# Kernel optimization log

Hardware: AMD Instinct MI355X
Metric: run time of the kernel (lower is better)

Reference implementation:

```python
import jax, jax.numpy as jnp
import numpy as np

GAMMA = 2.0
EPS = 1e-06
LAMBDA_DISTANCE = 1.0
LAMBDA_NORMAL = 0.01
LAMBDA_LAPLACIAN = 0.1
CLS = 1


def vertex_normals(v, f, eps=EPS):
    # v: [N,3], f: [F,3] int. Scatter face normals to vertices, then normalize.
    fv = v[f]  # [F,3,3]
    fn = jnp.cross(fv[:, 1] - fv[:, 0], fv[:, 2] - fv[:, 0])  # [F,3]
    vn = jnp.zeros_like(v)
    vn = vn.at[f[:, 0]].add(fn).at[f[:, 1]].add(fn).at[f[:, 2]].add(fn)
    norm = jnp.maximum(jnp.linalg.norm(vn, axis=-1, keepdims=True), eps)
    return vn / norm


def squared_cdist(a, b):
    # [Na,3] x [Nb,3] -> squared euclidean distances [Na,Nb] (clamped >= 0)
    a2 = jnp.sum(a * a, axis=1)[:, None]
    b2 = jnp.sum(b * b, axis=1)[None, :]
    d2 = a2 + b2 - 2.0 * (a @ b.T)
    return jnp.maximum(d2, 0.0)


def sample_binary_targets(label, v, cls=CLS):
    # Nearest-neighbor grid_sample, align_corners=True, padding zeros.
    # grid = 2*v - 1 -> voxel index = round(v * (size-1)); v[:,0]->W, v[:,1]->H, v[:,2]->D.
    D, H, W = label.shape[2], label.shape[3], label.shape[4]
    ix = jnp.round(v[:, 0] * (W - 1)).astype(jnp.int32)
    iy = jnp.round(v[:, 1] * (H - 1)).astype(jnp.int32)
    iz = jnp.round(v[:, 2] * (D - 1)).astype(jnp.int32)
    inb = (ix >= 0) & (ix < W) & (iy >= 0) & (iy < H) & (iz >= 0) & (iz < D)
    ixc = jnp.clip(ix, 0, W - 1)
    iyc = jnp.clip(iy, 0, H - 1)
    izc = jnp.clip(iz, 0, D - 1)
    vals = (label[0, 0, izc, iyc, ixc] == cls).astype(jnp.float32)
    return jnp.where(inb, vals, 0.0)


def spatial_consistency_loss(rel_pos, targets, gamma=GAMMA, eps=EPS):
    p = jnp.clip(rel_pos, eps, 1.0 - eps)
    pos = targets > 0.5
    pc = jnp.sum(pos).astype(p.dtype)
    tot = jnp.asarray(p.shape[0], p.dtype)
    nc = tot - pc
    alpha = nc / (tot + eps)
    lpos = -alpha * jnp.power(1.0 - p, gamma) * jnp.log(p)
    lneg = -(1.0 - alpha) * jnp.power(p, gamma) * jnp.log(1.0 - p)
    return jnp.sum(jnp.where(pos, lpos, lneg)) / (tot + eps)


def laplacian_uniform(v, f):
    # Uniform mesh Laplacian smoothing: || mean(neighbors) - v ||, averaged.
    i = jnp.concatenate([f[:, 0], f[:, 1], f[:, 2], f[:, 1], f[:, 2], f[:, 0]])
    j = jnp.concatenate([f[:, 1], f[:, 2], f[:, 0], f[:, 0], f[:, 1], f[:, 2]])
    nsum = jnp.zeros_like(v).at[i].add(v[j])
    deg = jnp.zeros((v.shape[0],), v.dtype).at[i].add(1.0)
    lap = nsum / jnp.maximum(deg, 1.0)[:, None] - v
    return jnp.mean(jnp.linalg.norm(lap, axis=1))


def loss_forward(pred_vertices, relative_positions, gt_vertices, pred_faces, gt_faces, label):
    gt_v = jax.lax.stop_gradient(gt_vertices)  # gt comes from label volume; detached in original
    gt_normals = vertex_normals(gt_v, gt_faces)
    # spatial (focal-style) loss
    targets = sample_binary_targets(label, pred_vertices)
    spatial = spatial_consistency_loss(relative_positions, targets)
    # chamfer-style squared surface distance
    d2 = squared_cdist(pred_vertices, gt_v)  # [Np,Ng]
    distance = jnp.mean(jnp.min(d2, axis=1)) + jnp.mean(jnp.min(d2, axis=0))
    # normal consistency vs nearest gt vertex
    pred_normals = vertex_normals(pred_vertices, pred_faces)
    nearest = jnp.argmin(d2, axis=1)
    normal = jnp.mean((pred_normals - gt_normals[nearest]) ** 2)
    # uniform laplacian smoothing
    laplacian = laplacian_uniform(pred_vertices, pred_faces)
    total = spatial + LAMBDA_DISTANCE * distance + LAMBDA_NORMAL * normal + LAMBDA_LAPLACIAN * laplacian
    return total


def setup_inputs() -> dict:
    key = jax.random.key(0)
    k1, k2, k3, k4, k5, k6 = jax.random.split(key, 6)
    Np, Ng = 8192, 12000
    pred_vertices = jax.random.uniform(k1, (Np, 3), dtype=jnp.float32)
    relative_positions = jax.random.uniform(k2, (Np,), dtype=jnp.float32)
    gt_vertices = jax.random.uniform(k3, (Ng, 3), dtype=jnp.float32)
    pred_faces = jax.random.randint(k4, (2 * Np, 3), 0, Np, dtype=jnp.int32)
    gt_faces = jax.random.randint(k5, (2 * Ng, 3), 0, Ng, dtype=jnp.int32)
    label = jax.random.randint(k6, (1, 1, 96, 96, 96), 0, 2, dtype=jnp.int32)
    return {"pred_vertices": pred_vertices, "relative_positions": relative_positions,
            "gt_vertices": gt_vertices, "pred_faces": pred_faces,
            "gt_faces": gt_faces, "label": label}


def reference(pred_vertices, relative_positions, gt_vertices, pred_faces, gt_faces, label):
    return loss_forward(pred_vertices, relative_positions, gt_vertices, pred_faces, gt_faces, label)
```

## Files before the change

### kernel.cpp

```cpp
#include <hip/hip_runtime.h>
#include <math.h>

#define NP 8192
#define NG 12000
#define NFP 16384
#define NFG 24000
#define EPSF 1e-6f

static constexpr size_t OFF_ROWMIN = 0;
static constexpr size_t OFF_COLMIN = 65536;
static constexpr size_t OFF_GTN    = 113664;
static constexpr size_t OFF_PNN    = 257664;
static constexpr size_t OFF_NSUM   = 355968;
static constexpr size_t OFF_DEG    = 454272;
static constexpr size_t OFF_SCAL   = 487040;
#define N_ZERO 93352

__global__ __launch_bounds__(256) void init_kernel(unsigned long long* __restrict__ rowmin,
                                                   unsigned* __restrict__ colmin,
                                                   float* __restrict__ zero) {
    int i = blockIdx.x * 256 + threadIdx.x;
    if (i < NP) rowmin[i] = 0xFFFFFFFFFFFFFFFFULL;
    if (i < NG) colmin[i] = 0x7f800000u;
    if (i < N_ZERO) zero[i] = 0.0f;
}

#define ROW_GROUPS 8
#define ROW_CHUNKS 64
#define ROW_CH 188
#define ROW_BLOCKS (ROW_GROUPS*ROW_CHUNKS)
#define COL_GROUPS 12
#define COL_CHUNKS 43
#define COL_CH 192
#define COL_BLOCKS (COL_GROUPS*COL_CHUNKS)
#define CD_BLOCKS (ROW_BLOCKS + COL_BLOCKS)
#define FACE_BLOCKS ((NFG + NFP + 255) / 256)

__global__ __launch_bounds__(256) void mega_kernel(const float* __restrict__ pred,
                                                   const int* __restrict__ pf,
                                                   const float* __restrict__ gt,
                                                   const int* __restrict__ gf,
                                                   unsigned long long* __restrict__ rowmin,
                                                   unsigned* __restrict__ colmin,
                                                   float* __restrict__ gtn,
                                                   float* __restrict__ pnn,
                                                   float* __restrict__ nsum,
                                                   float* __restrict__ deg) {
    __shared__ float4 s[COL_CH];
    int b = blockIdx.x;
    if (b < ROW_BLOCKS) {
        int group = b >> 6;
        int chunk = b & 63;
        int gbase = chunk * ROW_CH;
        for (int j = threadIdx.x; j < ROW_CH; j += 256) {
            int gj = gbase + j;
            if (gj < NG) {
                float x = gt[3*gj], y = gt[3*gj+1], z = gt[3*gj+2];
                s[j] = make_float4(x, y, z, fmaf(x,x, fmaf(y,y, z*z)));
            } else {
                s[j] = make_float4(0.f, 0.f, 0.f, 3.0e38f);
            }
        }
        __syncthreads();
        int pv0 = group * 1024 + threadIdx.x;
        float cx[4], cy[4], cz[4], a2[4], best[4];
        int bi[4];
        #pragma unroll
        for (int k = 0; k < 4; ++k) {
            int pv = pv0 + 256*k;
            float x = pred[3*pv], y = pred[3*pv+1], z = pred[3*pv+2];
            a2[k] = fmaf(x,x, fmaf(y,y, z*z));
            cx[k] = -2.0f*x; cy[k] = -2.0f*y; cz[k] = -2.0f*z;
            best[k] = 3.0e38f; bi[k] = 0;
        }
        #pragma unroll 4
        for (int j = 0; j < ROW_CH; ++j) {
            float4 q = s[j];
            #pragma unroll
            for (int k = 0; k < 4; ++k) {
                float t = fmaf(cx[k], q.x, fmaf(cy[k], q.y, fmaf(cz[k], q.z, q.w)));
                if (t < best[k]) { best[k] = t; bi[k] = gbase + j; }
            }
        }
        #pragma unroll
        for (int k = 0; k < 4; ++k) {
            float d2 = fmaxf(a2[k] + best[k], 0.0f);
            unsigned long long key =
                ((unsigned long long)__float_as_uint(d2) << 32) | (unsigned)bi[k];
            atomicMin(&rowmin[pv0 + 256*k], key);
        }
    } else if (b < CD_BLOCKS) {
        int bb = b - ROW_BLOCKS;
        int group = bb / COL_CHUNKS;
        int chunk = bb % COL_CHUNKS;
        int pbase = chunk * COL_CH;
        for (int j = threadIdx.x; j < COL_CH; j += 256) {
            int pj = pbase + j;
            if (pj < NP) {
                float x = pred[3*pj], y = pred[3*pj+1], z = pred[3*pj+2];
                s[j] = make_float4(x, y, z, fmaf(x,x, fmaf(y,y, z*z)));
            } else {
                s[j] = make_float4(0.f, 0.f, 0.f, 3.0e38f);
            }
        }
        __syncthreads();
        int gv0 = group * 1024 + threadIdx.x;
        float cx[4], cy[4], cz[4], a2[4], best[4];
        #pragma unroll
        for (int k = 0; k < 4; ++k) {
            int gv = gv0 + 256*k;
            float x = 0.f, y = 0.f, z = 0.f;
            if (gv < NG) { x = gt[3*gv]; y = gt[3*gv+1]; z = gt[3*gv+2]; }
            a2[k] = fmaf(x,x, fmaf(y,y, z*z));
            cx[k] = -2.0f*x; cy[k] = -2.0f*y; cz[k] = -2.0f*z;
            best[k] = 3.0e38f;
        }
        #pragma unroll 4
        for (int j = 0; j < COL_CH; ++j) {
            float4 q = s[j];
            #pragma unroll
            for (int k = 0; k < 4; ++k) {
                float t = fmaf(cx[k], q.x, fmaf(cy[k], q.y, fmaf(cz[k], q.z, q.w)));
                best[k] = fminf(best[k], t);
            }
        }
        #pragma unroll
        for (int k = 0; k < 4; ++k) {
            int gv = gv0 + 256*k;
            if (gv < NG) {
                float d2 = fmaxf(a2[k] + best[k], 0.0f);
                atomicMin(&colmin[gv], __float_as_uint(d2));
            }
        }
    } else {
        int t = (b - CD_BLOCKS) * 256 + threadIdx.x;
        if (t < NFG) {
            int i0 = gf[3*t], i1 = gf[3*t+1], i2 = gf[3*t+2];
            float ax = gt[3*i0], ay = gt[3*i0+1], az = gt[3*i0+2];
            float bx = gt[3*i1], by = gt[3*i1+1], bz = gt[3*i1+2];
            float cx = gt[3*i2], cy = gt[3*i2+1], cz = gt[3*i2+2];
            float ux = bx-ax, uy = by-ay, uz = bz-az;
            float wx = cx-ax, wy = cy-ay, wz = cz-az;
            float nx = uy*wz - uz*wy, ny = uz*wx - ux*wz, nz = ux*wy - uy*wx;
            atomicAdd(&gtn[3*i0+0], nx); atomicAdd(&gtn[3*i0+1], ny); atomicAdd(&gtn[3*i0+2], nz);
            atomicAdd(&gtn[3*i1+0], nx); atomicAdd(&gtn[3*i1+1], ny); atomicAdd(&gtn[3*i1+2], nz);
            atomicAdd(&gtn[3*i2+0], nx); atomicAdd(&gtn[3*i2+1], ny); atomicAdd(&gtn[3*i2+2], nz);
        } else if (t < NFG + NFP) {
            int u = t - NFG;
            int i0 = pf[3*u], i1 = pf[3*u+1], i2 = pf[3*u+2];
            float ax = pred[3*i0], ay = pred[3*i0+1], az = pred[3*i0+2];
            float bx = pred[3*i1], by = pred[3*i1+1], bz = pred[3*i1+2];
            float cx = pred[3*i2], cy = pred[3*i2+1], cz = pred[3*i2+2];
            float ux = bx-ax, uy = by-ay, uz = bz-az;
            float wx = cx-ax, wy = cy-ay, wz = cz-az;
            float nx = uy*wz - uz*wy, ny = uz*wx - ux*wz, nz = ux*wy - uy*wx;
            atomicAdd(&pnn[3*i0+0], nx); atomicAdd(&pnn[3*i0+1], ny); atomicAdd(&pnn[3*i0+2], nz);
            atomicAdd(&pnn[3*i1+0], nx); atomicAdd(&pnn[3*i1+1], ny); atomicAdd(&pnn[3*i1+2], nz);
            atomicAdd(&pnn[3*i2+0], nx); atomicAdd(&pnn[3*i2+1], ny); atomicAdd(&pnn[3*i2+2], nz);
            atomicAdd(&nsum[3*i0+0], bx+cx); atomicAdd(&nsum[3*i0+1], by+cy); atomicAdd(&nsum[3*i0+2], bz+cz);
            atomicAdd(&nsum[3*i1+0], cx+ax); atomicAdd(&nsum[3*i1+1], cy+ay); atomicAdd(&nsum[3*i1+2], cz+az);
            atomicAdd(&nsum[3*i2+0], ax+bx); atomicAdd(&nsum[3*i2+1], ay+by); atomicAdd(&nsum[3*i2+2], az+bz);
            atomicAdd(&deg[i0], 2.0f); atomicAdd(&deg[i1], 2.0f); atomicAdd(&deg[i2], 2.0f);
        }
    }
}

__device__ __forceinline__ float wave_sum(float x) {
    #pragma unroll
    for (int o = 32; o > 0; o >>= 1) x += __shfl_down(x, o, 64);
    return x;
}

#define FIN_PRED_BLOCKS 32
#define FIN_COL_BLOCKS 47
#define FIN_TOTAL (FIN_PRED_BLOCKS + FIN_COL_BLOCKS)
__global__ __launch_bounds__(256) void finalize_kernel(const float* __restrict__ pred,
                                                       const float* __restrict__ relpos,
                                                       const int* __restrict__ label,
                                                       const unsigned long long* __restrict__ rowmin,
                                                       const unsigned* __restrict__ colmin,
                                                       const float* __restrict__ pnn,
                                                       const float* __restrict__ gtn,
                                                       const float* __restrict__ nsum,
                                                       const float* __restrict__ deg,
                                                       float* __restrict__ scal,
                                                       unsigned* __restrict__ ticket,
                                                       float* __restrict__ out) {
    if (blockIdx.x < FIN_PRED_BLOCKS) {
        int v = blockIdx.x * 256 + threadIdx.x;
        unsigned long long key = rowmin[v];
        float dmin = __uint_as_float((unsigned)(key >> 32));
        int nearest = (int)(unsigned)(key & 0xffffffffu);
        float px = pred[3*v], py = pred[3*v+1], pz = pred[3*v+2];

        float ax = pnn[3*v], ay = pnn[3*v+1], az = pnn[3*v+2];
        float an = fmaxf(sqrtf(ax*ax + ay*ay + az*az), EPSF);
        float gx = gtn[3*nearest], gy = gtn[3*nearest+1], gz = gtn[3*nearest+2];
        float gn = fmaxf(sqrtf(gx*gx + gy*gy + gz*gz), EPSF);
        float nx = ax/an - gx/gn, ny = ay/an - gy/gn, nz = az/an - gz/gn;
        float sse = nx*nx + ny*ny + nz*nz;

        float d = fmaxf(deg[v], 1.0f);
        float lx = nsum[3*v]/d - px, ly = nsum[3*v+1]/d - py, lz = nsum[3*v+2]/d - pz;
        float lapn = sqrtf(lx*lx + ly*ly + lz*lz);

        int ix = (int)rintf(px * 95.0f), iy = (int)rintf(py * 95.0f), iz = (int)rintf(pz * 95.0f);
        bool inb = (ix >= 0) & (ix < 96) & (iy >= 0) & (iy < 96) & (iz >= 0) & (iz < 96);
        int ixc = min(max(ix, 0), 95), iyc = min(max(iy, 0), 95), izc = min(max(iz, 0), 95);
        bool pos = inb && (label[(izc*96 + iyc)*96 + ixc] == 1);

        float p = fminf(fmaxf(relpos[v], EPSF), 1.0f - EPSF);
        float om = 1.0f - p;
        float pcnt = 0.0f, sx = 0.0f, sy = 0.0f;
        if (pos) { pcnt = 1.0f; sx = om*om*logf(p); }
        else     { sy = p*p*logf(om); }

        float r0 = wave_sum(dmin);
        float r1 = wave_sum(sse);
        float r2 = wave_sum(lapn);
        float r3 = wave_sum(pcnt);
        float r4 = wave_sum(sx);
        float r5 = wave_sum(sy);
        if ((threadIdx.x & 63) == 0) {
            atomicAdd(&scal[0], r0);
            atomicAdd(&scal[5], r1);
            atomicAdd(&scal[6], r2);
            atomicAdd(&scal[2], r3);
            atomicAdd(&scal[3], r4);
            atomicAdd(&scal[4], r5);
        }
    } else {
        int gv = (blockIdx.x - FIN_PRED_BLOCKS) * 256 + threadIdx.x;
        float val = (gv < NG) ? __uint_as_float(colmin[gv]) : 0.0f;
        float r = wave_sum(val);
        if ((threadIdx.x & 63) == 0) atomicAdd(&scal[1], r);
    }

    __threadfence();
    __shared__ int is_last;
    if (threadIdx.x == 0) {
        unsigned t = atomicAdd(ticket, 1u);
        is_last = (t == FIN_TOTAL - 1) ? 1 : 0;
    }
    __syncthreads();
    if (is_last && threadIdx.x == 0) {
        float sum_row = atomicAdd(&scal[0], 0.0f);
        float sum_col = atomicAdd(&scal[1], 0.0f);
        float pc      = atomicAdd(&scal[2], 0.0f);
        float SX      = atomicAdd(&scal[3], 0.0f);
        float SY      = atomicAdd(&scal[4], 0.0f);
        float sse     = atomicAdd(&scal[5], 0.0f);
        float lap     = atomicAdd(&scal[6], 0.0f);
        float tot = (float)NP;
        float alpha = (tot - pc) / (tot + EPSF);
        float spatial = (-alpha * SX - (1.0f - alpha) * SY) / (tot + EPSF);
        float distance = sum_row / (float)NP + sum_col / (float)NG;
        float normal = sse / (float)(NP * 3);
        float lapm = lap / (float)NP;
        out[0] = spatial + 1.0f * distance + 0.01f * normal + 0.1f * lapm;
    }
}

extern "C" void kernel_launch(void* const* d_in, const int* in_sizes, int n_in,
                              void* d_out, int out_size, void* d_ws, size_t ws_size,
                              hipStream_t stream) {
    const float* pred   = (const float*)d_in[0];
    const float* relpos = (const float*)d_in[1];
    const float* gt     = (const float*)d_in[2];
    const int*   pfaces = (const int*)d_in[3];
    const int*   gfaces = (const int*)d_in[4];
    const int*   label  = (const int*)d_in[5];
    float* out = (float*)d_out;

    char* ws = (char*)d_ws;
    unsigned long long* rowmin = (unsigned long long*)(ws + OFF_ROWMIN);
    unsigned*           colmin = (unsigned*)(ws + OFF_COLMIN);
    float*              gtn    = (float*)(ws + OFF_GTN);
    float*              pnn    = (float*)(ws + OFF_PNN);
    float*              nsum   = (float*)(ws + OFF_NSUM);
    float*              deg    = (float*)(ws + OFF_DEG);
    float*              scal   = (float*)(ws + OFF_SCAL);
    unsigned*           ticket = (unsigned*)(ws + OFF_SCAL + 7*sizeof(float));

    hipLaunchKernelGGL(init_kernel, dim3((N_ZERO + 255) / 256), dim3(256), 0, stream,
                       rowmin, colmin, gtn);
    hipLaunchKernelGGL(mega_kernel, dim3(CD_BLOCKS + FACE_BLOCKS), dim3(256), 0, stream,
                       pred, pfaces, gt, gfaces, rowmin, colmin, gtn, pnn, nsum, deg);
    hipLaunchKernelGGL(finalize_kernel, dim3(FIN_TOTAL), dim3(256), 0, stream,
                       pred, relpos, label, rowmin, colmin, pnn, gtn, nsum, deg,
                       scal, ticket, out);
}
```

Measured before the change: 120.2 us.

## Replace atomicMin chamfer reduction with per-chunk partial buffers reduced in finalize

The chamfer row/column kernels now write per-chunk partial minima into large workspace buffers instead of doing global atomicMin, and the finalize kernel scans all chunks to reduce them. Each thread also handles 8 query points instead of 4 while the shared chunk is halved, which raises register reuse per shared-memory load. The init kernel no longer has to initialise the min buffers. In exchange, finalize reads about 12 MB of partial results, and the higher register count may lower occupancy.

New measurement: 134.6 us. 1.12x slower.

```diff
diff --git a/kernel.cpp b/kernel.cpp
--- a/kernel.cpp
+++ b/kernel.cpp
@@ -7,41 +7,38 @@
 #define NFG 24000
 #define EPSF 1e-6f
 
-static constexpr size_t OFF_ROWMIN = 0;
-static constexpr size_t OFF_COLMIN = 65536;
-static constexpr size_t OFF_GTN    = 113664;
-static constexpr size_t OFF_PNN    = 257664;
-static constexpr size_t OFF_NSUM   = 355968;
-static constexpr size_t OFF_DEG    = 454272;
-static constexpr size_t OFF_SCAL   = 487040;
-#define N_ZERO 93352
-
-__global__ __launch_bounds__(256) void init_kernel(unsigned long long* __restrict__ rowmin,
-                                                   unsigned* __restrict__ colmin,
-                                                   float* __restrict__ zero) {
-    int i = blockIdx.x * 256 + threadIdx.x;
-    if (i < NP) rowmin[i] = 0xFFFFFFFFFFFFFFFFULL;
-    if (i < NG) colmin[i] = 0x7f800000u;
-    if (i < N_ZERO) zero[i] = 0.0f;
-}
-
-#define ROW_GROUPS 8
-#define ROW_CHUNKS 64
-#define ROW_CH 188
+#define ROW_GROUPS 4
+#define ROW_CHUNKS 128
+#define ROW_CH 94
 #define ROW_BLOCKS (ROW_GROUPS*ROW_CHUNKS)
-#define COL_GROUPS 12
-#define COL_CHUNKS 43
-#define COL_CH 192
+#define COL_GROUPS 6
+#define COL_CHUNKS 86
+#define COL_CH 96
 #define COL_BLOCKS (COL_GROUPS*COL_CHUNKS)
 #define CD_BLOCKS (ROW_BLOCKS + COL_BLOCKS)
 #define FACE_BLOCKS ((NFG + NFP + 255) / 256)
+#define NGPAD (COL_GROUPS*2048)
+
+static constexpr size_t OFF_ROWPART = 0;
+static constexpr size_t OFF_COLPART = 8388608;
+static constexpr size_t OFF_GTN     = 12615680;
+static constexpr size_t OFF_PNN     = 12759680;
+static constexpr size_t OFF_NSUM    = 12857984;
+static constexpr size_t OFF_DEG     = 12956288;
+static constexpr size_t OFF_SCAL    = 12989056;
+#define N_ZERO 93352
+
+__global__ __launch_bounds__(256) void init_kernel(float* __restrict__ zero) {
+    int i = blockIdx.x * 256 + threadIdx.x;
+    if (i < N_ZERO) zero[i] = 0.0f;
+}
 
 __global__ __launch_bounds__(256) void mega_kernel(const float* __restrict__ pred,
                                                    const int* __restrict__ pf,
                                                    const float* __restrict__ gt,
                                                    const int* __restrict__ gf,
-                                                   unsigned long long* __restrict__ rowmin,
-                                                   unsigned* __restrict__ colmin,
+                                                   unsigned long long* __restrict__ rowpart,
+                                                   float* __restrict__ colpart,
                                                    float* __restrict__ gtn,
                                                    float* __restrict__ pnn,
                                                    float* __restrict__ nsum,
@@ -49,9 +46,20 @@
     __shared__ float4 s[COL_CH];
     int b = blockIdx.x;
     if (b < ROW_BLOCKS) {
-        int group = b >> 6;
-        int chunk = b & 63;
+        int group = b >> 7;
+        int chunk = b & 127;
         int gbase = chunk * ROW_CH;
+        int pv0 = group * 2048 + threadIdx.x;
+        float cx[8], cy[8], cz[8], a2[8], best[8];
+        int bi[8];
+        #pragma unroll
+        for (int k = 0; k < 8; ++k) {
+            int pv = pv0 + 256*k;
+            float x = pred[3*pv], y = pred[3*pv+1], z = pred[3*pv+2];
+            a2[k] = fmaf(x,x, fmaf(y,y, z*z));
+            cx[k] = -2.0f*x; cy[k] = -2.0f*y; cz[k] = -2.0f*z;
+            best[k] = 3.0e38f; bi[k] = 0;
+        }
         for (int j = threadIdx.x; j < ROW_CH; j += 256) {
             int gj = gbase + j;
             if (gj < NG) {
@@ -62,38 +70,37 @@
             }
         }
         __syncthreads();
-        int pv0 = group * 1024 + threadIdx.x;
-        float cx[4], cy[4], cz[4], a2[4], best[4];
-        int bi[4];
-        #pragma unroll
-        for (int k = 0; k < 4; ++k) {
-            int pv = pv0 + 256*k;
-            float x = pred[3*pv], y = pred[3*pv+1], z = pred[3*pv+2];
-            a2[k] = fmaf(x,x, fmaf(y,y, z*z));
-            cx[k] = -2.0f*x; cy[k] = -2.0f*y; cz[k] = -2.0f*z;
-            best[k] = 3.0e38f; bi[k] = 0;
-        }
-        #pragma unroll 4
+        #pragma unroll 2
         for (int j = 0; j < ROW_CH; ++j) {
             float4 q = s[j];
             #pragma unroll
-            for (int k = 0; k < 4; ++k) {
+            for (int k = 0; k < 8; ++k) {
                 float t = fmaf(cx[k], q.x, fmaf(cy[k], q.y, fmaf(cz[k], q.z, q.w)));
-                if (t < best[k]) { best[k] = t; bi[k] = gbase + j; }
-            }
-        }
-        #pragma unroll
-        for (int k = 0; k < 4; ++k) {
+                if (t < best[k]) { best[k] = t; bi[k] = j; }
+            }
+        }
+        #pragma unroll
+        for (int k = 0; k < 8; ++k) {
             float d2 = fmaxf(a2[k] + best[k], 0.0f);
-            unsigned long long key =
-                ((unsigned long long)__float_as_uint(d2) << 32) | (unsigned)bi[k];
-            atomicMin(&rowmin[pv0 + 256*k], key);
+            rowpart[(size_t)chunk * NP + pv0 + 256*k] =
+                ((unsigned long long)__float_as_uint(d2) << 32) | (unsigned)(gbase + bi[k]);
         }
     } else if (b < CD_BLOCKS) {
         int bb = b - ROW_BLOCKS;
         int group = bb / COL_CHUNKS;
         int chunk = bb % COL_CHUNKS;
         int pbase = chunk * COL_CH;
+        int gv0 = group * 2048 + threadIdx.x;
+        float cx[8], cy[8], cz[8], a2[8], best[8];
+        #pragma unroll
+        for (int k = 0; k < 8; ++k) {
+            int gv = gv0 + 256*k;
+            float x = 0.f, y = 0.f, z = 0.f;
+            if (gv < NG) { x = gt[3*gv]; y = gt[3*gv+1]; z = gt[3*gv+2]; }
+            a2[k] = fmaf(x,x, fmaf(y,y, z*z));
+            cx[k] = -2.0f*x; cy[k] = -2.0f*y; cz[k] = -2.0f*z;
+            best[k] = 3.0e38f;
+        }
         for (int j = threadIdx.x; j < COL_CH; j += 256) {
             int pj = pbase + j;
             if (pj < NP) {
@@ -104,33 +111,19 @@
             }
         }
         __syncthreads();
-        int gv0 = group * 1024 + threadIdx.x;
-        float cx[4], cy[4], cz[4], a2[4], best[4];
-        #pragma unroll
-        for (int k = 0; k < 4; ++k) {
-            int gv = gv0 + 256*k;
-            float x = 0.f, y = 0.f, z = 0.f;
-            if (gv < NG) { x = gt[3*gv]; y = gt[3*gv+1]; z = gt[3*gv+2]; }
-            a2[k] = fmaf(x,x, fmaf(y,y, z*z));
-            cx[k] = -2.0f*x; cy[k] = -2.0f*y; cz[k] = -2.0f*z;
-            best[k] = 3.0e38f;
-        }
-        #pragma unroll 4
+        #pragma unroll 2
         for (int j = 0; j < COL_CH; ++j) {
             float4 q = s[j];
             #pragma unroll
-            for (int k = 0; k < 4; ++k) {
+            for (int k = 0; k < 8; ++k) {
                 float t = fmaf(cx[k], q.x, fmaf(cy[k], q.y, fmaf(cz[k], q.z, q.w)));
                 best[k] = fminf(best[k], t);
             }
         }
         #pragma unroll
-        for (int k = 0; k < 4; ++k) {
-            int gv = gv0 + 256*k;
-            if (gv < NG) {
-                float d2 = fmaxf(a2[k] + best[k], 0.0f);
-                atomicMin(&colmin[gv], __float_as_uint(d2));
-            }
+        for (int k = 0; k < 8; ++k) {
+            float d2 = fmaxf(a2[k] + best[k], 0.0f);
+            colpart[(size_t)chunk * NGPAD + gv0 + 256*k] = d2;
         }
     } else {
         int t = (b - CD_BLOCKS) * 256 + threadIdx.x;
@@ -172,13 +165,13 @@
 }
 
 #define FIN_PRED_BLOCKS 32
-#define FIN_COL_BLOCKS 47
+#define FIN_COL_BLOCKS 48
 #define FIN_TOTAL (FIN_PRED_BLOCKS + FIN_COL_BLOCKS)
 __global__ __launch_bounds__(256) void finalize_kernel(const float* __restrict__ pred,
                                                        const float* __restrict__ relpos,
                                                        const int* __restrict__ label,
-                                                       const unsigned long long* __restrict__ rowmin,
-                                                       const unsigned* __restrict__ colmin,
+                                                       const unsigned long long* __restrict__ rowpart,
+                                                       const float* __restrict__ colpart,
                                                        const float* __restrict__ pnn,
                                                        const float* __restrict__ gtn,
                                                        const float* __restrict__ nsum,
@@ -188,7 +181,12 @@
                                                        float* __restrict__ out) {
     if (blockIdx.x < FIN_PRED_BLOCKS) {
         int v = blockIdx.x * 256 + threadIdx.x;
-        unsigned long long key = rowmin[v];
+        unsigned long long key = 0xFFFFFFFFFFFFFFFFULL;
+        #pragma unroll 4
+        for (int c = 0; c < ROW_CHUNKS; ++c) {
+            unsigned long long k2 = rowpart[(size_t)c * NP + v];
+            key = (k2 < key) ? k2 : key;
+        }
         float dmin = __uint_as_float((unsigned)(key >> 32));
         int nearest = (int)(unsigned)(key & 0xffffffffu);
         float px = pred[3*v], py = pred[3*v+1], pz = pred[3*v+2];
@@ -231,7 +229,11 @@
         }
     } else {
         int gv = (blockIdx.x - FIN_PRED_BLOCKS) * 256 + threadIdx.x;
-        float val = (gv < NG) ? __uint_as_float(colmin[gv]) : 0.0f;
+        float best = 3.4e38f;
+        #pragma unroll 4
+        for (int c = 0; c < COL_CHUNKS; ++c)
+            best = fminf(best, colpart[(size_t)c * NGPAD + gv]);
+        float val = (gv < NG) ? best : 0.0f;
         float r = wave_sum(val);
         if ((threadIdx.x & 63) == 0) atomicAdd(&scal[1], r);
     }
@@ -273,20 +275,20 @@
     float* out = (float*)d_out;
 
     char* ws = (char*)d_ws;
-    unsigned long long* rowmin = (unsigned long long*)(ws + OFF_ROWMIN);
-    unsigned*           colmin = (unsigned*)(ws + OFF_COLMIN);
-    float*              gtn    = (float*)(ws + OFF_GTN);
-    float*              pnn    = (float*)(ws + OFF_PNN);
-    float*              nsum   = (float*)(ws + OFF_NSUM);
-    float*              deg    = (float*)(ws + OFF_DEG);
-    float*              scal   = (float*)(ws + OFF_SCAL);
-    unsigned*           ticket = (unsigned*)(ws + OFF_SCAL + 7*sizeof(float));
+    unsigned long long* rowpart = (unsigned long long*)(ws + OFF_ROWPART);
+    float*              colpart = (float*)(ws + OFF_COLPART);
+    float*              gtn     = (float*)(ws + OFF_GTN);
+    float*              pnn     = (float*)(ws + OFF_PNN);
+    float*              nsum    = (float*)(ws + OFF_NSUM);
+    float*              deg     = (float*)(ws + OFF_DEG);
+    float*              scal    = (float*)(ws + OFF_SCAL);
+    unsigned*           ticket  = (unsigned*)(ws + OFF_SCAL + 7*sizeof(float));
 
     hipLaunchKernelGGL(init_kernel, dim3((N_ZERO + 255) / 256), dim3(256), 0, stream,
-                       rowmin, colmin, gtn);
+                       gtn);
     hipLaunchKernelGGL(mega_kernel, dim3(CD_BLOCKS + FACE_BLOCKS), dim3(256), 0, stream,
-                       pred, pfaces, gt, gfaces, rowmin, colmin, gtn, pnn, nsum, deg);
+                       pred, pfaces, gt, gfaces, rowpart, colpart, gtn, pnn, nsum, deg);
     hipLaunchKernelGGL(finalize_kernel, dim3(FIN_TOTAL), dim3(256), 0, stream,
-                       pred, relpos, label, rowmin, colmin, pnn, gtn, nsum, deg,
+                       pred, relpos, label, rowpart, colpart, pnn, gtn, nsum, deg,
                        scal, ticket, out);
 }
```

## Replace brute-force Chamfer distance with uniform grid nearest-neighbor search

Applied to the files above, without the earlier changes.

Replaces the all-pairs squared-distance min reductions with a 16^3 uniform grid. A single block builds cell histograms and prefix sums, a scatter pass buckets points into cell-sorted float4 arrays, and the finalize kernel queries each point by expanding Chebyshev shells until a distance bound proves the best is final. This removes O(Np*Ng) distance work at the cost of a serial single-block build, atomic scatter with nondeterministic order within cells, and divergent per-thread search loops. It relies on the coordinates being roughly uniform in [0,1].

Result: slower. 172.2 us (+43.3%).

```diff
diff --git a/kernel.cpp b/kernel.cpp
--- a/kernel.cpp
+++ b/kernel.cpp
@@ -7,133 +7,122 @@
 #define NFG 24000
 #define EPSF 1e-6f
 
-static constexpr size_t OFF_ROWMIN = 0;
-static constexpr size_t OFF_COLMIN = 65536;
-static constexpr size_t OFF_GTN    = 113664;
-static constexpr size_t OFF_PNN    = 257664;
-static constexpr size_t OFF_NSUM   = 355968;
-static constexpr size_t OFF_DEG    = 454272;
-static constexpr size_t OFF_SCAL   = 487040;
+#define GR 16
+#define NC (GR*GR*GR)
+#define HCELL 0.0625f
+
+static constexpr size_t OFF_STARTP = 0;
+static constexpr size_t OFF_CURP   = 16384;
+static constexpr size_t OFF_STARTG = 32768;
+static constexpr size_t OFF_CURG   = 49152;
+static constexpr size_t OFF_SORTP  = 65536;
+static constexpr size_t OFF_SORTG  = 196608;
+static constexpr size_t OFF_GTN    = 388608;
+static constexpr size_t OFF_PNN    = 532608;
+static constexpr size_t OFF_NSUM   = 630912;
+static constexpr size_t OFF_DEG    = 729216;
+static constexpr size_t OFF_SCAL   = 761984;
+static constexpr size_t OFF_TICKET = 762012;
 #define N_ZERO 93352
 
-__global__ __launch_bounds__(256) void init_kernel(unsigned long long* __restrict__ rowmin,
-                                                   unsigned* __restrict__ colmin,
-                                                   float* __restrict__ zero) {
-    int i = blockIdx.x * 256 + threadIdx.x;
-    if (i < NP) rowmin[i] = 0xFFFFFFFFFFFFFFFFULL;
-    if (i < NG) colmin[i] = 0x7f800000u;
-    if (i < N_ZERO) zero[i] = 0.0f;
-}
-
-#define ROW_GROUPS 8
-#define ROW_CHUNKS 64
-#define ROW_CH 188
-#define ROW_BLOCKS (ROW_GROUPS*ROW_CHUNKS)
-#define COL_GROUPS 12
-#define COL_CHUNKS 43
-#define COL_CH 192
-#define COL_BLOCKS (COL_GROUPS*COL_CHUNKS)
-#define CD_BLOCKS (ROW_BLOCKS + COL_BLOCKS)
+__device__ __forceinline__ int cell_of(float x) {
+    int c = (int)(x * (float)GR);
+    return min(max(c, 0), GR - 1);
+}
+
+__global__ __launch_bounds__(1024) void build_kernel(const float* __restrict__ pred,
+                                                     const float* __restrict__ gt,
+                                                     unsigned* __restrict__ startP,
+                                                     unsigned* __restrict__ curP,
+                                                     unsigned* __restrict__ startG,
+                                                     unsigned* __restrict__ curG,
+                                                     float* __restrict__ zero) {
+    if (blockIdx.x == 0) {
+        __shared__ unsigned hP[NC];
+        __shared__ unsigned hG[NC];
+        __shared__ unsigned ps[1024];
+        int t = threadIdx.x;
+        for (int i = t; i < NC; i += 1024) { hP[i] = 0u; hG[i] = 0u; }
+        __syncthreads();
+        for (int i = t; i < NP; i += 1024) {
+            int c = (cell_of(pred[3*i+2]) * GR + cell_of(pred[3*i+1])) * GR + cell_of(pred[3*i]);
+            atomicAdd(&hP[c], 1u);
+        }
+        for (int i = t; i < NG; i += 1024) {
+            int c = (cell_of(gt[3*i+2]) * GR + cell_of(gt[3*i+1])) * GR + cell_of(gt[3*i]);
+            atomicAdd(&hG[c], 1u);
+        }
+        __syncthreads();
+        {
+            unsigned a0 = hP[4*t], a1 = hP[4*t+1], a2 = hP[4*t+2], a3 = hP[4*t+3];
+            unsigned tsum = a0 + a1 + a2 + a3;
+            ps[t] = tsum; __syncthreads();
+            for (int off = 1; off < 1024; off <<= 1) {
+                unsigned v = (t >= off) ? ps[t - off] : 0u;
+                __syncthreads();
+                ps[t] += v;
+                __syncthreads();
+            }
+            unsigned ex = ps[t] - tsum;
+            hP[4*t] = ex; hP[4*t+1] = ex + a0; hP[4*t+2] = ex + a0 + a1; hP[4*t+3] = ex + a0 + a1 + a2;
+            __syncthreads();
+            for (int i = t; i < NC; i += 1024) { startP[i] = hP[i]; curP[i] = hP[i]; }
+            __syncthreads();
+        }
+        {
+            unsigned a0 = hG[4*t], a1 = hG[4*t+1], a2 = hG[4*t+2], a3 = hG[4*t+3];
+            unsigned tsum = a0 + a1 + a2 + a3;
+            ps[t] = tsum; __syncthreads();
+            for (int off = 1; off < 1024; off <<= 1) {
+                unsigned v = (t >= off) ? ps[t - off] : 0u;
+                __syncthreads();
+                ps[t] += v;
+                __syncthreads();
+            }
+            unsigned ex = ps[t] - tsum;
+            hG[4*t] = ex; hG[4*t+1] = ex + a0; hG[4*t+2] = ex + a0 + a1; hG[4*t+3] = ex + a0 + a1 + a2;
+            __syncthreads();
+            for (int i = t; i < NC; i += 1024) { startG[i] = hG[i]; curG[i] = hG[i]; }
+        }
+    } else {
+        int i = (blockIdx.x - 1) * 1024 + threadIdx.x;
+        if (i < N_ZERO) zero[i] = 0.0f;
+    }
+}
+
+#define SCAT_P_BLOCKS 32
+#define SCAT_G_BLOCKS 47
+#define SCAT_BLOCKS (SCAT_P_BLOCKS + SCAT_G_BLOCKS)
 #define FACE_BLOCKS ((NFG + NFP + 255) / 256)
-
-__global__ __launch_bounds__(256) void mega_kernel(const float* __restrict__ pred,
-                                                   const int* __restrict__ pf,
-                                                   const float* __restrict__ gt,
-                                                   const int* __restrict__ gf,
-                                                   unsigned long long* __restrict__ rowmin,
-                                                   unsigned* __restrict__ colmin,
-                                                   float* __restrict__ gtn,
-                                                   float* __restrict__ pnn,
-                                                   float* __restrict__ nsum,
-                                                   float* __restrict__ deg) {
-    __shared__ float4 s[COL_CH];
+__global__ __launch_bounds__(256) void scatter_faces_kernel(const float* __restrict__ pred,
+                                                            const int* __restrict__ pf,
+                                                            const float* __restrict__ gt,
+                                                            const int* __restrict__ gf,
+                                                            unsigned* __restrict__ curP,
+                                                            unsigned* __restrict__ curG,
+                                                            float4* __restrict__ sortP,
+                                                            float4* __restrict__ sortG,
+                                                            float* __restrict__ gtn,
+                                                            float* __restrict__ pnn,
+                                                            float* __restrict__ nsum,
+                                                            float* __restrict__ deg) {
     int b = blockIdx.x;
-    if (b < ROW_BLOCKS) {
-        int group = b >> 6;
-        int chunk = b & 63;
-        int gbase = chunk * ROW_CH;
-        for (int j = threadIdx.x; j < ROW_CH; j += 256) {
-            int gj = gbase + j;
-            if (gj < NG) {
-                float x = gt[3*gj], y = gt[3*gj+1], z = gt[3*gj+2];
-                s[j] = make_float4(x, y, z, fmaf(x,x, fmaf(y,y, z*z)));
-            } else {
-                s[j] = make_float4(0.f, 0.f, 0.f, 3.0e38f);
-            }
-        }
-        __syncthreads();
-        int pv0 = group * 1024 + threadIdx.x;
-        float cx[4], cy[4], cz[4], a2[4], best[4];
-        int bi[4];
-        #pragma unroll
-        for (int k = 0; k < 4; ++k) {
-            int pv = pv0 + 256*k;
-            float x = pred[3*pv], y = pred[3*pv+1], z = pred[3*pv+2];
-            a2[k] = fmaf(x,x, fmaf(y,y, z*z));
-            cx[k] = -2.0f*x; cy[k] = -2.0f*y; cz[k] = -2.0f*z;
-            best[k] = 3.0e38f; bi[k] = 0;
-        }
-        #pragma unroll 4
-        for (int j = 0; j < ROW_CH; ++j) {
-            float4 q = s[j];
-            #pragma unroll
-            for (int k = 0; k < 4; ++k) {
-                float t = fmaf(cx[k], q.x, fmaf(cy[k], q.y, fmaf(cz[k], q.z, q.w)));
-                if (t < best[k]) { best[k] = t; bi[k] = gbase + j; }
-            }
-        }
-        #pragma unroll
-        for (int k = 0; k < 4; ++k) {
-            float d2 = fmaxf(a2[k] + best[k], 0.0f);
-            unsigned long long key =
-                ((unsigned long long)__float_as_uint(d2) << 32) | (unsigned)bi[k];
-            atomicMin(&rowmin[pv0 + 256*k], key);
-        }
-    } else if (b < CD_BLOCKS) {
-        int bb = b - ROW_BLOCKS;
-        int group = bb / COL_CHUNKS;
-        int chunk = bb % COL_CHUNKS;
-        int pbase = chunk * COL_CH;
-        for (int j = threadIdx.x; j < COL_CH; j += 256) {
-            int pj = pbase + j;
-            if (pj < NP) {
-                float x = pred[3*pj], y = pred[3*pj+1], z = pred[3*pj+2];
-                s[j] = make_float4(x, y, z, fmaf(x,x, fmaf(y,y, z*z)));
-            } else {
-                s[j] = make_float4(0.f, 0.f, 0.f, 3.0e38f);
-            }
-        }
-        __syncthreads();
-        int gv0 = group * 1024 + threadIdx.x;
-        float cx[4], cy[4], cz[4], a2[4], best[4];
-        #pragma unroll
-        for (int k = 0; k < 4; ++k) {
-            int gv = gv0 + 256*k;
-            float x = 0.f, y = 0.f, z = 0.f;
-            if (gv < NG) { x = gt[3*gv]; y = gt[3*gv+1]; z = gt[3*gv+2]; }
-            a2[k] = fmaf(x,x, fmaf(y,y, z*z));
-            cx[k] = -2.0f*x; cy[k] = -2.0f*y; cz[k] = -2.0f*z;
-            best[k] = 3.0e38f;
-        }
-        #pragma unroll 4
-        for (int j = 0; j < COL_CH; ++j) {
-            float4 q = s[j];
-            #pragma unroll
-            for (int k = 0; k < 4; ++k) {
-                float t = fmaf(cx[k], q.x, fmaf(cy[k], q.y, fmaf(cz[k], q.z, q.w)));
-                best[k] = fminf(best[k], t);
-            }
-        }
-        #pragma unroll
-        for (int k = 0; k < 4; ++k) {
-            int gv = gv0 + 256*k;
-            if (gv < NG) {
-                float d2 = fmaxf(a2[k] + best[k], 0.0f);
-                atomicMin(&colmin[gv], __float_as_uint(d2));
-            }
+    if (b < SCAT_P_BLOCKS) {
+        int i = b * 256 + threadIdx.x;
+        float x = pred[3*i], y = pred[3*i+1], z = pred[3*i+2];
+        int c = (cell_of(z) * GR + cell_of(y)) * GR + cell_of(x);
+        unsigned pos = atomicAdd(&curP[c], 1u);
+        sortP[pos] = make_float4(x, y, z, __int_as_float(i));
+    } else if (b < SCAT_BLOCKS) {
+        int i = (b - SCAT_P_BLOCKS) * 256 + threadIdx.x;
+        if (i < NG) {
+            float x = gt[3*i], y = gt[3*i+1], z = gt[3*i+2];
+            int c = (cell_of(z) * GR + cell_of(y)) * GR + cell_of(x);
+            unsigned pos = atomicAdd(&curG[c], 1u);
+            sortG[pos] = make_float4(x, y, z, __int_as_float(i));
         }
     } else {
-        int t = (b - CD_BLOCKS) * 256 + threadIdx.x;
+        int t = (b - SCAT_BLOCKS) * 256 + threadIdx.x;
         if (t < NFG) {
             int i0 = gf[3*t], i1 = gf[3*t+1], i2 = gf[3*t+2];
             float ax = gt[3*i0], ay = gt[3*i0+1], az = gt[3*i0+2];
@@ -171,27 +160,82 @@
     return x;
 }
 
+__device__ __forceinline__ void grid_nn(float px, float py, float pz,
+                                        const float4* __restrict__ S,
+                                        const unsigned* __restrict__ cstart,
+                                        const unsigned* __restrict__ cend,
+                                        bool track_idx,
+                                        float& best_out, int& bi_out) {
+    int cx = cell_of(px), cy = cell_of(py), cz = cell_of(pz);
+    float best = 3.0e38f;
+    int bi = 0x7fffffff;
+    for (int r = 0; r < GR; ++r) {
+        int zlo = max(cz - r, 0), zhi = min(cz + r, GR - 1);
+        int ylo = max(cy - r, 0), yhi = min(cy + r, GR - 1);
+        int xlo = max(cx - r, 0), xhi = min(cx + r, GR - 1);
+        for (int z = zlo; z <= zhi; ++z) {
+            int az = abs(z - cz);
+            for (int y = ylo; y <= yhi; ++y) {
+                int ay = abs(y - cy);
+                for (int x = xlo; x <= xhi; ++x) {
+                    int ax = abs(x - cx);
+                    int cheb = max(ax, max(ay, az));
+                    if (cheb != r) continue;
+                    int c = (z * GR + y) * GR + x;
+                    unsigned s0 = cstart[c], s1 = cend[c];
+                    for (unsigned t = s0; t < s1; ++t) {
+                        float4 q = S[t];
+                        float dx = px - q.x, dy = py - q.y, dz = pz - q.z;
+                        float d2 = fmaf(dx, dx, fmaf(dy, dy, dz*dz));
+                        int qi = __float_as_int(q.w);
+                        if (d2 < best || (track_idx && d2 == best && qi < bi)) {
+                            best = d2; bi = qi;
+                        }
+                    }
+                }
+            }
+        }
+        if (best < 3.0e38f) {
+            float blo = 1.0e30f;
+            if (cx - r > 0)      blo = fminf(blo, px - (float)(cx - r) * HCELL);
+            if (cx + r < GR - 1) blo = fminf(blo, (float)(cx + r + 1) * HCELL - px);
+            if (cy - r > 0)      blo = fminf(blo, py - (float)(cy - r) * HCELL);
+            if (cy + r < GR - 1) blo = fminf(blo, (float)(cy + r + 1) * HCELL - py);
+            if (cz - r > 0)      blo = fminf(blo, pz - (float)(cz - r) * HCELL);
+            if (cz + r < GR - 1) blo = fminf(blo, (float)(cz + r + 1) * HCELL - pz);
+            if (blo >= 1.0e29f || best <= blo * blo) break;
+        }
+    }
+    best_out = best;
+    bi_out = bi;
+}
+
 #define FIN_PRED_BLOCKS 32
 #define FIN_COL_BLOCKS 47
 #define FIN_TOTAL (FIN_PRED_BLOCKS + FIN_COL_BLOCKS)
-__global__ __launch_bounds__(256) void finalize_kernel(const float* __restrict__ pred,
-                                                       const float* __restrict__ relpos,
-                                                       const int* __restrict__ label,
-                                                       const unsigned long long* __restrict__ rowmin,
-                                                       const unsigned* __restrict__ colmin,
-                                                       const float* __restrict__ pnn,
-                                                       const float* __restrict__ gtn,
-                                                       const float* __restrict__ nsum,
-                                                       const float* __restrict__ deg,
-                                                       float* __restrict__ scal,
-                                                       unsigned* __restrict__ ticket,
-                                                       float* __restrict__ out) {
+__global__ __launch_bounds__(256) void query_finalize_kernel(const float* __restrict__ relpos,
+                                                             const int* __restrict__ label,
+                                                             const float4* __restrict__ sortP,
+                                                             const float4* __restrict__ sortG,
+                                                             const unsigned* __restrict__ startP,
+                                                             const unsigned* __restrict__ endP,
+                                                             const unsigned* __restrict__ startG,
+                                                             const unsigned* __restrict__ endG,
+                                                             const float* __restrict__ pnn,
+                                                             const float* __restrict__ gtn,
+                                                             const float* __restrict__ nsum,
+                                                             const float* __restrict__ deg,
+                                                             float* __restrict__ scal,
+                                                             unsigned* __restrict__ ticket,
+                                                             float* __restrict__ out) {
     if (blockIdx.x < FIN_PRED_BLOCKS) {
-        int v = blockIdx.x * 256 + threadIdx.x;
-        unsigned long long key = rowmin[v];
-        float dmin = __uint_as_float((unsigned)(key >> 32));
-        int nearest = (int)(unsigned)(key & 0xffffffffu);
-        float px = pred[3*v], py = pred[3*v+1], pz = pred[3*v+2];
+        int i = blockIdx.x * 256 + threadIdx.x;
+        float4 P = sortP[i];
+        int v = __float_as_int(P.w);
+        float px = P.x, py = P.y, pz = P.z;
+
+        float dmin; int nearest;
+        grid_nn(px, py, pz, sortG, startG, endG, true, dmin, nearest);
 
         float ax = pnn[3*v], ay = pnn[3*v+1], az = pnn[3*v+2];
         float an = fmaxf(sqrtf(ax*ax + ay*ay + az*az), EPSF);
@@ -230,8 +274,14 @@
             atomicAdd(&scal[4], r5);
         }
     } else {
-        int gv = (blockIdx.x - FIN_PRED_BLOCKS) * 256 + threadIdx.x;
-        float val = (gv < NG) ? __uint_as_float(colmin[gv]) : 0.0f;
+        int i = (blockIdx.x - FIN_PRED_BLOCKS) * 256 + threadIdx.x;
+        float val = 0.0f;
+        if (i < NG) {
+            float4 Q = sortG[i];
+            float dmin; int dummy;
+            grid_nn(Q.x, Q.y, Q.z, sortP, startP, endP, false, dmin, dummy);
+            val = dmin;
+        }
         float r = wave_sum(val);
         if ((threadIdx.x & 63) == 0) atomicAdd(&scal[1], r);
     }
@@ -273,20 +323,26 @@
     float* out = (float*)d_out;
 
     char* ws = (char*)d_ws;
-    unsigned long long* rowmin = (unsigned long long*)(ws + OFF_ROWMIN);
-    unsigned*           colmin = (unsigned*)(ws + OFF_COLMIN);
-    float*              gtn    = (float*)(ws + OFF_GTN);
-    float*              pnn    = (float*)(ws + OFF_PNN);
-    float*              nsum   = (float*)(ws + OFF_NSUM);
-    float*              deg    = (float*)(ws + OFF_DEG);
-    float*              scal   = (float*)(ws + OFF_SCAL);
-    unsigned*           ticket = (unsigned*)(ws + OFF_SCAL + 7*sizeof(float));
-
-    hipLaunchKernelGGL(init_kernel, dim3((N_ZERO + 255) / 256), dim3(256), 0, stream,
-                       rowmin, colmin, gtn);
-    hipLaunchKernelGGL(mega_kernel, dim3(CD_BLOCKS + FACE_BLOCKS), dim3(256), 0, stream,
-                       pred, pfaces, gt, gfaces, rowmin, colmin, gtn, pnn, nsum, deg);
-    hipLaunchKernelGGL(finalize_kernel, dim3(FIN_TOTAL), dim3(256), 0, stream,
-                       pred, relpos, label, rowmin, colmin, pnn, gtn, nsum, deg,
-                       scal, ticket, out);
-}
+    unsigned* startP = (unsigned*)(ws + OFF_STARTP);
+    unsigned* curP   = (unsigned*)(ws + OFF_CURP);
+    unsigned* startG = (unsigned*)(ws + OFF_STARTG);
+    unsigned* curG   = (unsigned*)(ws + OFF_CURG);
+    float4*   sortP  = (float4*)(ws + OFF_SORTP);
+    float4*   sortG  = (float4*)(ws + OFF_SORTG);
+    float*    gtn    = (float*)(ws + OFF_GTN);
+    float*    pnn    = (float*)(ws + OFF_PNN);
+    float*    nsum   = (float*)(ws + OFF_NSUM);
+    float*    deg    = (float*)(ws + OFF_DEG);
+    float*    scal   = (float*)(ws + OFF_SCAL);
+    unsigned* ticket = (unsigned*)(ws + OFF_TICKET);
+
+    int zero_blocks = (N_ZERO + 1023) / 1024;
+    hipLaunchKernelGGL(build_kernel, dim3(1 + zero_blocks), dim3(1024), 0, stream,
+                       pred, gt, startP, curP, startG, curG, gtn);
+    hipLaunchKernelGGL(scatter_faces_kernel, dim3(SCAT_BLOCKS + FACE_BLOCKS), dim3(256), 0, stream,
+                       pred, pfaces, gt, gfaces, curP, curG, sortP, sortG,
+                       gtn, pnn, nsum, deg);
+    hipLaunchKernelGGL(query_finalize_kernel, dim3(FIN_TOTAL), dim3(256), 0, stream,
+                       relpos, label, sortP, sortG, startP, curP, startG, curG,
+                       pnn, gtn, nsum, deg, scal, ticket, out);
+}
```
